# Kernel optimization log

Hardware: AMD Instinct MI355X
Metric: run time of the kernel (lower is better)

Reference implementation:

```python
import jax, jax.numpy as jnp
import numpy as np

FEAT = 128
BATCH = 4
T_VAL = 256
TAU_VAL = 256
N_NODES = T_VAL + TAU_VAL
NUM_SAMPLES = 5


def _linear_init(key, fan_in, fan_out):
    s = 1.0 / np.sqrt(fan_in)
    kw, kb = jax.random.split(key)
    W = jax.random.uniform(kw, (fan_in, fan_out), minval=-s, maxval=s, dtype=jnp.float32)
    b = jax.random.uniform(kb, (fan_out,), minval=-s, maxval=s, dtype=jnp.float32)
    return W, b


def setup_inputs() -> dict:
    key = jax.random.key(0)
    k0, k1, k2, k3 = jax.random.split(key, 4)
    W1, b1 = _linear_init(k0, 2 * FEAT, FEAT)
    W2, b2 = _linear_init(k1, FEAT, FEAT)
    W3, b3 = _linear_init(k2, FEAT, 1)
    nodes = jax.random.normal(k3, (BATCH, N_NODES, FEAT), dtype=jnp.float32)
    return dict(
        nodes=nodes,
        W1=W1, b1=b1, g1=jnp.ones((FEAT,), jnp.float32), be1=jnp.zeros((FEAT,), jnp.float32),
        W2=W2, b2=b2, g2=jnp.ones((FEAT,), jnp.float32), be2=jnp.zeros((FEAT,), jnp.float32),
        W3=W3, b3=b3,
        T=T_VAL, taus=TAU_VAL, B=BATCH,
    )


def _layernorm(h, g, b):
    mu = h.mean(-1, keepdims=True)
    var = ((h - mu) ** 2).mean(-1, keepdims=True)
    return (h - mu) / jnp.sqrt(var + 1e-5) * g + b


def reference(nodes, W1, b1, g1, be1, W2, b2, g2, be2, W3, b3, T, taus, B):
    N = nodes.shape[1]  # = T + taus
    # Static tril edge structure (uniform T, taus across batch): rows=sink, cols=source
    rows, cols = np.tril_indices(N, -1)
    keep = rows > T  # strictly greater, as in the torch code
    sink_idx = jnp.asarray(rows[keep])   # [E]
    src_idx = jnp.asarray(cols[keep])    # [E]
    E = sink_idx.shape[0]

    # Gather node pairs -> [B, E, 2F]
    net_in = jnp.concatenate([nodes[:, sink_idx], nodes[:, src_idx]], axis=-1)

    # Small MLP: Linear-ReLU-LN x2 + Linear -> logits [B, E]
    h = _layernorm(jax.nn.relu(net_in @ W1 + b1), g1, be1)
    h = _layernorm(jax.nn.relu(h @ W2 + b2), g2, be2)
    logits = (h @ W3 + b3)[..., 0]

    # Gumbel-softmax (hard, tau=1) over edges, NUM_SAMPLES samples per batch
    gkey = jax.random.key(42)
    gnoise = jax.random.gumbel(gkey, (logits.shape[0], NUM_SAMPLES, E), dtype=logits.dtype)
    y_soft = jax.nn.softmax(logits[:, None, :] + gnoise, axis=-1)  # [B, S, E]
    y_hard = jax.nn.one_hot(jnp.argmax(y_soft, axis=-1), E, dtype=y_soft.dtype)
    y = y_hard + y_soft - jax.lax.stop_gradient(y_soft)  # straight-through hard sample

    counts = y.sum(axis=1)  # [B, E], in [0, S]
    # StraightThroughEstimator: forward binarize >0, identity gradient
    path = (counts > 0).astype(counts.dtype) + counts - jax.lax.stop_gradient(counts)

    # Scatter into dense adjacency (dense form of the sparse COO output)
    bidx = jnp.arange(nodes.shape[0])[:, None]
    adj = jnp.zeros((nodes.shape[0], N, N), nodes.dtype)
    adj = adj.at[bidx, sink_idx[None, :], src_idx[None, :]].set(path)
    return adj
```

## Files before the change

kernel.cpp:

```cpp
#include <hip/hip_runtime.h>
#include <stdint.h>

#define FEAT 128
#define NNODES 512
#define BATCH 4
#define EDGES 97920
#define BE (BATCH*EDGES)
#define NSAMP 5
#define BASE_OFF 32896
#define CHUNKS 40
#define NWT (BE/32)
#define MLP_GRID 510
#define MAP_BLOCKS 383
#define PREP_BLOCKS 64
#define VEC_BLOCK (256 + MAP_BLOCKS + PREP_BLOCKS)
#define ZERO_BLOCKS 256
#define SETUP_GRID (VEC_BLOCK + 1 + ZERO_BLOCKS)

typedef float f32x4 __attribute__((ext_vector_type(4)));
typedef short s16x8 __attribute__((ext_vector_type(8)));

__device__ __forceinline__ void threefry2x32(uint32_t k0, uint32_t k1,
                                             uint32_t& x0, uint32_t& x1) {
  uint32_t k2 = k0 ^ k1 ^ 0x1BD11BDAu;
  x0 += k0; x1 += k1;
#define RR(r) { x0 += x1; x1 = (x1 << (r)) | (x1 >> (32 - (r))); x1 ^= x0; }
  RR(13) RR(15) RR(26) RR(6)   x0 += k1; x1 += k2 + 1u;
  RR(17) RR(29) RR(16) RR(24)  x0 += k2; x1 += k0 + 2u;
  RR(13) RR(15) RR(26) RR(6)   x0 += k0; x1 += k1 + 3u;
  RR(17) RR(29) RR(16) RR(24)  x0 += k1; x1 += k2 + 4u;
  RR(13) RR(15) RR(26) RR(6)   x0 += k2; x1 += k0 + 5u;
#undef RR
}

__device__ __forceinline__ float gumbel_valf(uint32_t n) {
  uint32_t x0 = 0u, x1 = n;
  threefry2x32(0u, 42u, x0, x1);
  uint32_t bits = x0 ^ x1;
  uint32_t fb = (bits >> 9) | 0x3f800000u;
  float f = __uint_as_float(fb) - 1.0f;
  float u = fmaxf(f, 1.1754943508222875e-38f);
  return -logf(-logf(u));
}

template <int CTRL>
__device__ __forceinline__ float dpp_ror_add(float v) {
  int t = __builtin_amdgcn_update_dpp(0, __float_as_int(v), CTRL, 0xF, 0xF, true);
  return v + __int_as_float(t);
}
__device__ __forceinline__ float row_sum16(float v) {
  v = dpp_ror_add<0x128>(v);
  v = dpp_ror_add<0x124>(v);
  v = dpp_ror_add<0x122>(v);
  v = dpp_ror_add<0x121>(v);
  return v;
}

__global__ __launch_bounds__(256) void setup_kernel(
    const float* __restrict__ nodes, const float* __restrict__ W1,
    const float* __restrict__ b1, const float* __restrict__ W2,
    const float* __restrict__ g1, const float* __restrict__ be1,
    const float* __restrict__ b2, const float* __restrict__ g2,
    const float* __restrict__ be2, const float* __restrict__ W3,
    const float* __restrict__ b3, float* __restrict__ P, float* __restrict__ Q,
    int2* __restrict__ map, unsigned short* __restrict__ GFH,
    unsigned short* __restrict__ GFL, float* __restrict__ SG,
    float* __restrict__ SB, float* __restrict__ GW3, float* __restrict__ SC,
    float* __restrict__ adj) {
  const int blk = blockIdx.x;
  const int tid = threadIdx.x;
  if (blk < 256) {
    __shared__ float snode[8][FEAT];
    const int row0 = blk * 8;
    for (int i = tid; i < 8 * FEAT; i += 256)
      snode[i >> 7][i & 127] = nodes[row0 * FEAT + i];
    __syncthreads();
    const int j = tid & 127;
    const int half = tid >> 7;
    const float* w = W1 + half * FEAT * FEAT + j;
    float acc[8] = {0, 0, 0, 0, 0, 0, 0, 0};
    for (int k4 = 0; k4 < 32; ++k4) {
      const float* wp = w + (k4 * 4) * FEAT;
      const float w0 = wp[0], w1 = wp[FEAT], w2 = wp[2 * FEAT], w3 = wp[3 * FEAT];
#pragma unroll
      for (int m = 0; m < 8; ++m) {
        const float4 nv = *(const float4*)&snode[m][k4 * 4];
        acc[m] = fmaf(nv.x, w0, acc[m]);
        acc[m] = fmaf(nv.y, w1, acc[m]);
        acc[m] = fmaf(nv.z, w2, acc[m]);
        acc[m] = fmaf(nv.w, w3, acc[m]);
      }
    }
    const float bv = half ? 0.0f : b1[j];
    float* out = half ? Q : P;
#pragma unroll
    for (int m = 0; m < 8; ++m) out[(row0 + m) * FEAT + j] = acc[m] + bv;
  } else if (blk < 256 + MAP_BLOCKS) {
    int e = (blk - 256) * 256 + tid;
    if (e < EDGES) {
      double x = (double)(e + BASE_OFF);
      int s = (int)((1.0 + sqrt(1.0 + 8.0 * x)) * 0.5);
      while ((long long)s * (s - 1) / 2 - BASE_OFF > e) --s;
      while ((long long)(s + 1) * s / 2 - BASE_OFF <= e) ++s;
      int src = e - (int)((long long)s * (s - 1) / 2 - BASE_OFF);
      map[e] = make_int2(s, src);
    }
  } else if (blk < VEC_BLOCK) {
    const int idx = (blk - (256 + MAP_BLOCKS)) * 256 + tid;
    const int j = idx & 7;
    const int lane = (idx >> 3) & 63;
    const int nt = (idx >> 9) & 7;
    const int kt = (idx >> 12) & 3;
    const int n = nt * 16 + (lane & 15);
    const int k = kt * 32 + ((lane >> 4) << 3) + j;
    const float g = g1[k] * W2[k * FEAT + n];
    const uint32_t gu = __float_as_uint(g);
    const float d = g - __uint_as_float(gu & 0xFFFF0000u);
    GFH[idx] = (unsigned short)(gu >> 16);
    GFL[idx] = (unsigned short)(__float_as_uint(d) >> 16);
  } else if (blk == VEC_BLOCK) {
    __shared__ float partS[256], partB[256], rg[128], rb[128];
    {
      const int n = tid & 127, kh = tid >> 7;
      float sg = 0.f, sb = 0.f;
      const int k0 = kh * 64;
#pragma unroll 8
      for (int k = k0; k < k0 + 64; ++k) {
        const float w = W2[k * FEAT + n];
        sg = fmaf(g1[k], w, sg);
        sb = fmaf(be1[k], w, sb);
      }
      partS[tid] = sg;
      partB[tid] = sb;
    }
    __syncthreads();
    if (tid < 128) {
      SG[tid] = partS[tid] + partS[tid + 128];
      SB[tid] = partB[tid] + partB[tid + 128] + b2[tid];
      const float gw = g2[tid] * W3[tid];
      GW3[tid] = gw;
      rg[tid] = gw;
      rb[tid] = be2[tid] * W3[tid];
    }
    __syncthreads();
    for (int off = 64; off; off >>= 1) {
      if (tid < off) { rg[tid] += rg[tid + off]; rb[tid] += rb[tid + off]; }
      __syncthreads();
    }
    if (tid == 0) { SC[0] = rg[0]; SC[1] = rb[0] + b3[0]; }
  } else {
    float4* a4 = (float4*)adj;
    const int base = (blk - (VEC_BLOCK + 1)) * 1024 + tid;
#pragma unroll
    for (int jj = 0; jj < 4; ++jj)
      a4[base + jj * 256] = make_float4(0.f, 0.f, 0.f, 0.f);
  }
}

__global__ __launch_bounds__(256, 2) void mlp_kernel(
    const float* __restrict__ P, const float* __restrict__ Q,
    const int2* __restrict__ map,
    const unsigned short* __restrict__ GFH,
    const unsigned short* __restrict__ GFL,
    const float* __restrict__ SG, const float* __restrict__ SB,
    const float* __restrict__ GW3, const float* __restrict__ SC,
    float* __restrict__ logits) {
  __shared__ s16x8 sBH[2048];
  __shared__ s16x8 sBL[2048];
  const int tid = threadIdx.x;
  const int lane = tid & 63;
  const int wave = tid >> 6;
  const int cl = lane & 15;
  const int qd = lane >> 4;

  {
    const float4* s1p = (const float4*)GFH;
    const float4* s2p = (const float4*)GFL;
    float4* d1 = (float4*)sBH;
    float4* d2 = (float4*)sBL;
    for (int i = tid; i < 2048; i += 256) { d1[i] = s1p[i]; d2[i] = s2p[i]; }
  }
  __syncthreads();

  const float sgw3 = SC[0], cb = SC[1];

#pragma unroll 1
  for (int it = 0; it < 6; ++it) {
    const int wt = blockIdx.x * 24 + it * 4 + wave;
    const int g0 = wt * 32;
    const int b = g0 / EDGES;
    const int e0 = g0 - b * EDGES;
    const int bofs = (b << 9);

    s16x8 Ah[2][4], Al[2][4];
    float s1v[2], q1v[2];
#pragma unroll
    for (int mt = 0; mt < 2; ++mt) {
      const int2 ss = map[e0 + mt * 16 + cl];
      const float* pr = P + ((size_t)(bofs + ss.x) << 7) + qd * 8;
      const float* qr = Q + ((size_t)(bofs + ss.y) << 7) + qd * 8;
      float s1 = 0.f, q1 = 0.f;
#pragma unroll
      for (int kt = 0; kt < 4; ++kt) {
        const float4 pa = *(const float4*)(pr + kt * 32);
        const float4 pb = *(const float4*)(pr + kt * 32 + 4);
        const float4 qa = *(const float4*)(qr + kt * 32);
        const float4 qb = *(const float4*)(qr + kt * 32 + 4);
        const float uu[8] = {
            fmaxf(pa.x + qa.x, 0.f), fmaxf(pa.y + qa.y, 0.f),
            fmaxf(pa.z + qa.z, 0.f), fmaxf(pa.w + qa.w, 0.f),
            fmaxf(pb.x + qb.x, 0.f), fmaxf(pb.y + qb.y, 0.f),
            fmaxf(pb.z + qb.z, 0.f), fmaxf(pb.w + qb.w, 0.f)};
#pragma unroll
        for (int j = 0; j < 8; ++j) {
          const float h = uu[j];
          s1 += h;
          q1 = fmaf(h, h, q1);
          const uint32_t xu = __float_as_uint(h);
          const float d = h - __uint_as_float(xu & 0xFFFF0000u);
          Ah[mt][kt][j] = (short)(xu >> 16);
          Al[mt][kt][j] = (short)(__float_as_uint(d) >> 16);
        }
      }
      s1v[mt] = s1;
      q1v[mt] = q1;
    }
    __builtin_amdgcn_sched_barrier(0);

    f32x4 acc[2][8];
#pragma unroll
    for (int mt = 0; mt < 2; ++mt)
#pragma unroll
      for (int nt = 0; nt < 8; ++nt) acc[mt][nt] = (f32x4){0.f, 0.f, 0.f, 0.f};

    s16x8 Bh[2][2], Bl[2][2];
#pragma unroll
    for (int s = 0; s < 2; ++s) {
      const int base = ((s >> 2) * 8 + (s & 3) * 2) * 64 + lane;
      Bh[s][0] = sBH[base];      Bl[s][0] = sBL[base];
      Bh[s][1] = sBH[base + 64]; Bl[s][1] = sBL[base + 64];
    }
#pragma unroll
    for (int g = 0; g < 16; ++g) {
      const int kt = g >> 2;
      const int n0 = (g & 3) * 2, n1 = n0 + 1;
      const int sl = g & 1;
      acc[0][n0] = __builtin_amdgcn_mfma_f32_16x16x32_bf16(Ah[0][kt], Bh[sl][0], acc[0][n0], 0, 0, 0);
      acc[1][n0] = __builtin_amdgcn_mfma_f32_16x16x32_bf16(Ah[1][kt], Bh[sl][0], acc[1][n0], 0, 0, 0);
      acc[0][n1] = __builtin_amdgcn_mfma_f32_16x16x32_bf16(Ah[0][kt], Bh[sl][1], acc[0][n1], 0, 0, 0);
      acc[1][n1] = __builtin_amdgcn_mfma_f32_16x16x32_bf16(Ah[1][kt], Bh[sl][1], acc[1][n1], 0, 0, 0);
      acc[0][n0] = __builtin_amdgcn_mfma_f32_16x16x32_bf16(Al[0][kt], Bh[sl][0], acc[0][n0], 0, 0, 0);
      acc[1][n0] = __builtin_amdgcn_mfma_f32_16x16x32_bf16(Al[1][kt], Bh[sl][0], acc[1][n0], 0, 0, 0);
      acc[0][n1] = __builtin_amdgcn_mfma_f32_16x16x32_bf16(Al[0][kt], Bh[sl][1], acc[0][n1], 0, 0, 0);
      acc[1][n1] = __builtin_amdgcn_mfma_f32_16x16x32_bf16(Al[1][kt], Bh[sl][1], acc[1][n1], 0, 0, 0);
      acc[0][n0] = __builtin_amdgcn_mfma_f32_16x16x32_bf16(Ah[0][kt], Bl[sl][0], acc[0][n0], 0, 0, 0);
      acc[1][n0] = __builtin_amdgcn_mfma_f32_16x16x32_bf16(Ah[1][kt], Bl[sl][0], acc[1][n0], 0, 0, 0);
      acc[0][n1] = __builtin_amdgcn_mfma_f32_16x16x32_bf16(Ah[0][kt], Bl[sl][1], acc[0][n1], 0, 0, 0);
      acc[1][n1] = __builtin_amdgcn_mfma_f32_16x16x32_bf16(Ah[1][kt], Bl[sl][1], acc[1][n1], 0, 0, 0);
      if (g < 14) {
        const int g2 = g + 2;
        const int base = ((g2 >> 2) * 8 + (g2 & 3) * 2) * 64 + lane;
        Bh[sl][0] = sBH[base];      Bl[sl][0] = sBL[base];
        Bh[sl][1] = sBH[base + 64]; Bl[sl][1] = sBL[base + 64];
      }
      __builtin_amdgcn_sched_barrier(0);
    }

    float mu[2], rs[2];
#pragma unroll
    for (int mt = 0; mt < 2; ++mt) {
      float s1 = s1v[mt], q1 = q1v[mt];
      s1 += __shfl_xor(s1, 16, 64);
      s1 += __shfl_xor(s1, 32, 64);
      q1 += __shfl_xor(q1, 16, 64);
      q1 += __shfl_xor(q1, 32, 64);
      mu[mt] = s1 * (1.0f / 128.0f);
      const float var = fmaxf(q1 * (1.0f / 128.0f) - mu[mt] * mu[mt], 0.0f);
      rs[mt] = rsqrtf(var + 1e-5f);
    }

    int zz;
    asm volatile("v_mov_b32 %0, 0" : "=v"(zz));
    float SGn[8], SBn[8], GWn[8];
#pragma unroll
    for (int nt = 0; nt < 8; ++nt) {
      const int n = nt * 16 + cl + zz;
      SGn[nt] = SG[n];
      SBn[nt] = SB[n];
      GWn[nt] = GW3[n];
    }
#pragma unroll
    for (int mt = 0; mt < 2; ++mt) {
#pragma unroll
      for (int r = 0; r < 4; ++r) {
        const int me = qd * 4 + r;
        const float mue = __shfl(mu[mt], me, 64);
        const float rse = __shfl(rs[mt], me, 64);
        float s2 = 0.f, q2 = 0.f, t = 0.f;
#pragma unroll
        for (int nt = 0; nt < 8; ++nt) {
          const float Sraw = acc[mt][nt][r];
          const float z = fmaf(rse, fmaf(-mue, SGn[nt], Sraw), SBn[nt]);
          const float h2 = fmaxf(z, 0.f);
          s2 += h2;
          q2 = fmaf(h2, h2, q2);
          t = fmaf(h2, GWn[nt], t);
        }
        s2 = row_sum16(s2);
        q2 = row_sum16(q2);
        t  = row_sum16(t);
        if (cl == 0) {
          const float mu2 = s2 * (1.0f / 128.0f);
          const float var2 = fmaxf(q2 * (1.0f / 128.0f) - mu2 * mu2, 0.0f);
          const float rs2 = rsqrtf(var2 + 1e-5f);
          logits[g0 + mt * 16 + me] = rs2 * (t - mu2 * sgw3) + cb;
        }
      }
    }
  }
}

__global__ __launch_bounds__(256) void gumbel_kernel(
    const float* __restrict__ logits, float* __restrict__ bestval,
    int* __restrict__ bestidx) {
  const int bs = blockIdx.x / CHUNKS;
  const int chunk = blockIdx.x % CHUNKS;
  const int b = bs / NSAMP;
  const float* lg = logits + b * EDGES;
  float best = -1e30f; int bi = 0x7fffffff;
  for (int e = chunk * 256 + threadIdx.x; e < EDGES; e += CHUNKS * 256) {
    uint32_t n = (uint32_t)(bs * EDGES + e);
    float val = lg[e] + gumbel_valf(n);
    if (val > best) { best = val; bi = e; }
  }
  __shared__ float sv[256];
  __shared__ int si[256];
  sv[threadIdx.x] = best; si[threadIdx.x] = bi;
  __syncthreads();
  for (int off = 128; off; off >>= 1) {
    if (threadIdx.x < off) {
      float ov = sv[threadIdx.x + off]; int oi = si[threadIdx.x + off];
      if (ov > sv[threadIdx.x] ||
          (ov == sv[threadIdx.x] && oi < si[threadIdx.x])) {
        sv[threadIdx.x] = ov; si[threadIdx.x] = oi;
      }
    }
    __syncthreads();
  }
  if (threadIdx.x == 0) { bestval[blockIdx.x] = sv[0]; bestidx[blockIdx.x] = si[0]; }
}

__global__ __launch_bounds__(64) void select_kernel(
    const float* __restrict__ bestval, const int* __restrict__ bestidx,
    const int2* __restrict__ map, float* __restrict__ adj) {
  const int bs = blockIdx.x;
  const int lane = threadIdx.x;
  float v = -1e30f; int idx = 0x7fffffff;
  if (lane < CHUNKS) { v = bestval[bs * CHUNKS + lane]; idx = bestidx[bs * CHUNKS + lane]; }
#pragma unroll
  for (int off = 32; off; off >>= 1) {
    float ov = __shfl_xor(v, off, 64);
    int oi = __shfl_xor(idx, off, 64);
    if (ov > v || (ov == v && oi < idx)) { v = ov; idx = oi; }
  }
  if (lane == 0) {
    int b = bs / NSAMP;
    int2 ss = map[idx];
    adj[((b * NNODES) + ss.x) * NNODES + ss.y] = 1.0f;
  }
}

extern "C" void kernel_launch(void* const* d_in, const int* in_sizes, int n_in,
                              void* d_out, int out_size, void* d_ws, size_t ws_size,
                              hipStream_t stream) {
  const float* nodes = (const float*)d_in[0];
  const float* W1  = (const float*)d_in[1];
  const float* b1  = (const float*)d_in[2];
  const float* g1  = (const float*)d_in[3];
  const float* be1 = (const float*)d_in[4];
  const float* W2  = (const float*)d_in[5];
  const float* b2  = (const float*)d_in[6];
  const float* g2  = (const float*)d_in[7];
  const float* be2 = (const float*)d_in[8];
  const float* W3  = (const float*)d_in[9];
  const float* b3  = (const float*)d_in[10];
  float* adj = (float*)d_out;

  char* ws = (char*)d_ws;
  float* P       = (float*)(ws);
  float* Q       = (float*)(ws + (1 << 20));
  int2*  map     = (int2*) (ws + (2 << 20));
  float* logits  = (float*)(ws + (3 << 20));
  unsigned short* GFH = (unsigned short*)(ws + (5 << 20));
  unsigned short* GFL = (unsigned short*)(ws + (5 << 20) + 32768);
  float* SG      = (float*)(ws + (5 << 20) + 65536);
  float* SB      = (float*)(ws + (5 << 20) + 66048);
  float* GW3     = (float*)(ws + (5 << 20) + 66560);
  float* SC      = (float*)(ws + (5 << 20) + 67072);
  float* bestval = (float*)(ws + (5 << 20) + 131072);
  int*   bestidx = (int*)  (ws + (5 << 20) + 137472);

  setup_kernel<<<SETUP_GRID, 256, 0, stream>>>(
      nodes, W1, b1, W2, g1, be1, b2, g2, be2, W3, b3,
      P, Q, map, GFH, GFL, SG, SB, GW3, SC, adj);
  mlp_kernel<<<MLP_GRID, 256, 0, stream>>>(P, Q, map, GFH, GFL,
                                           SG, SB, GW3, SC, logits);
  gumbel_kernel<<<20 * CHUNKS, 256, 0, stream>>>(logits, bestval, bestidx);
  select_kernel<<<20, 64, 0, stream>>>(bestval, bestidx, map, adj);
}
```

Baseline: 153.1 us.

## Shrink MLP wave tile to 16 edges, read low-part weights from global

Each wave now handles 16 edges per iteration instead of 32, with twice as many iterations per block. This halves the register footprint and allows occupancy hint 3. The low bf16 half of the weight matrix is no longer staged in LDS and is instead loaded directly from global memory, which halves shared memory use per block. The trade-off is less B-operand reuse per wave, since each weight fragment now feeds half as many MFMAs, plus extra global or L2 traffic for the low-part weights inside the MFMA loop.

Result: slower. 240.9 us (+57.4%).

```diff
diff --git a/kernel.cpp b/kernel.cpp
--- a/kernel.cpp
+++ b/kernel.cpp
@@ -9,7 +9,7 @@
 #define NSAMP 5
 #define BASE_OFF 32896
 #define CHUNKS 40
-#define NWT (BE/32)
+#define NWT (BE/16)
 #define MLP_GRID 510
 #define MAP_BLOCKS 383
 #define PREP_BLOCKS 64
@@ -157,7 +157,7 @@
   }
 }
 
-__global__ __launch_bounds__(256, 2) void mlp_kernel(
+__global__ __launch_bounds__(256, 3) void mlp_kernel(
     const float* __restrict__ P, const float* __restrict__ Q,
     const int2* __restrict__ map,
     const unsigned short* __restrict__ GFH,
@@ -166,7 +166,6 @@
     const float* __restrict__ GW3, const float* __restrict__ SC,
     float* __restrict__ logits) {
   __shared__ s16x8 sBH[2048];
-  __shared__ s16x8 sBL[2048];
   const int tid = threadIdx.x;
   const int lane = tid & 63;
   const int wave = tid >> 6;
@@ -175,31 +174,28 @@
 
   {
     const float4* s1p = (const float4*)GFH;
-    const float4* s2p = (const float4*)GFL;
     float4* d1 = (float4*)sBH;
-    float4* d2 = (float4*)sBL;
-    for (int i = tid; i < 2048; i += 256) { d1[i] = s1p[i]; d2[i] = s2p[i]; }
+    for (int i = tid; i < 2048; i += 256) d1[i] = s1p[i];
   }
   __syncthreads();
 
+  const s16x8* gfl = (const s16x8*)GFL;
   const float sgw3 = SC[0], cb = SC[1];
 
 #pragma unroll 1
-  for (int it = 0; it < 6; ++it) {
-    const int wt = blockIdx.x * 24 + it * 4 + wave;
-    const int g0 = wt * 32;
+  for (int it = 0; it < 12; ++it) {
+    const int wt = blockIdx.x * 48 + it * 4 + wave;
+    const int g0 = wt * 16;
     const int b = g0 / EDGES;
     const int e0 = g0 - b * EDGES;
     const int bofs = (b << 9);
 
-    s16x8 Ah[2][4], Al[2][4];
-    float s1v[2], q1v[2];
-#pragma unroll
-    for (int mt = 0; mt < 2; ++mt) {
-      const int2 ss = map[e0 + mt * 16 + cl];
+    s16x8 Ah[4], Al[4];
+    float s1 = 0.f, q1 = 0.f;
+    {
+      const int2 ss = map[e0 + cl];
       const float* pr = P + ((size_t)(bofs + ss.x) << 7) + qd * 8;
       const float* qr = Q + ((size_t)(bofs + ss.y) << 7) + qd * 8;
-      float s1 = 0.f, q1 = 0.f;
 #pragma unroll
       for (int kt = 0; kt < 4; ++kt) {
         const float4 pa = *(const float4*)(pr + kt * 32);
@@ -218,66 +214,51 @@
           q1 = fmaf(h, h, q1);
           const uint32_t xu = __float_as_uint(h);
           const float d = h - __uint_as_float(xu & 0xFFFF0000u);
-          Ah[mt][kt][j] = (short)(xu >> 16);
-          Al[mt][kt][j] = (short)(__float_as_uint(d) >> 16);
+          Ah[kt][j] = (short)(xu >> 16);
+          Al[kt][j] = (short)(__float_as_uint(d) >> 16);
         }
       }
-      s1v[mt] = s1;
-      q1v[mt] = q1;
     }
     __builtin_amdgcn_sched_barrier(0);
 
-    f32x4 acc[2][8];
-#pragma unroll
-    for (int mt = 0; mt < 2; ++mt)
-#pragma unroll
-      for (int nt = 0; nt < 8; ++nt) acc[mt][nt] = (f32x4){0.f, 0.f, 0.f, 0.f};
+    f32x4 acc[8];
+#pragma unroll
+    for (int nt = 0; nt < 8; ++nt) acc[nt] = (f32x4){0.f, 0.f, 0.f, 0.f};
 
     s16x8 Bh[2][2], Bl[2][2];
 #pragma unroll
     for (int s = 0; s < 2; ++s) {
       const int base = ((s >> 2) * 8 + (s & 3) * 2) * 64 + lane;
-      Bh[s][0] = sBH[base];      Bl[s][0] = sBL[base];
-      Bh[s][1] = sBH[base + 64]; Bl[s][1] = sBL[base + 64];
+      Bh[s][0] = sBH[base];      Bl[s][0] = gfl[base];
+      Bh[s][1] = sBH[base + 64]; Bl[s][1] = gfl[base + 64];
     }
 #pragma unroll
     for (int g = 0; g < 16; ++g) {
       const int kt = g >> 2;
       const int n0 = (g & 3) * 2, n1 = n0 + 1;
       const int sl = g & 1;
-      acc[0][n0] = __builtin_amdgcn_mfma_f32_16x16x32_bf16(Ah[0][kt], Bh[sl][0], acc[0][n0], 0, 0, 0);
-      acc[1][n0] = __builtin_amdgcn_mfma_f32_16x16x32_bf16(Ah[1][kt], Bh[sl][0], acc[1][n0], 0, 0, 0);
-      acc[0][n1] = __builtin_amdgcn_mfma_f32_16x16x32_bf16(Ah[0][kt], Bh[sl][1], acc[0][n1], 0, 0, 0);
-      acc[1][n1] = __builtin_amdgcn_mfma_f32_16x16x32_bf16(Ah[1][kt], Bh[sl][1], acc[1][n1], 0, 0, 0);
-      acc[0][n0] = __builtin_amdgcn_mfma_f32_16x16x32_bf16(Al[0][kt], Bh[sl][0], acc[0][n0], 0, 0, 0);
-      acc[1][n0] = __builtin_amdgcn_mfma_f32_16x16x32_bf16(Al[1][kt], Bh[sl][0], acc[1][n0], 0, 0, 0);
-      acc[0][n1] = __builtin_amdgcn_mfma_f32_16x16x32_bf16(Al[0][kt], Bh[sl][1], acc[0][n1], 0, 0, 0);
-      acc[1][n1] = __builtin_amdgcn_mfma_f32_16x16x32_bf16(Al[1][kt], Bh[sl][1], acc[1][n1], 0, 0, 0);
-      acc[0][n0] = __builtin_amdgcn_mfma_f32_16x16x32_bf16(Ah[0][kt], Bl[sl][0], acc[0][n0], 0, 0, 0);
-      acc[1][n0] = __builtin_amdgcn_mfma_f32_16x16x32_bf16(Ah[1][kt], Bl[sl][0], acc[1][n0], 0, 0, 0);
-      acc[0][n1] = __builtin_amdgcn_mfma_f32_16x16x32_bf16(Ah[0][kt], Bl[sl][1], acc[0][n1], 0, 0, 0);
-      acc[1][n1] = __builtin_amdgcn_mfma_f32_16x16x32_bf16(Ah[1][kt], Bl[sl][1], acc[1][n1], 0, 0, 0);
+      acc[n0] = __builtin_amdgcn_mfma_f32_16x16x32_bf16(Ah[kt], Bh[sl][0], acc[n0], 0, 0, 0);
+      acc[n1] = __builtin_amdgcn_mfma_f32_16x16x32_bf16(Ah[kt], Bh[sl][1], acc[n1], 0, 0, 0);
+      acc[n0] = __builtin_amdgcn_mfma_f32_16x16x32_bf16(Al[kt], Bh[sl][0], acc[n0], 0, 0, 0);
+      acc[n1] = __builtin_amdgcn_mfma_f32_16x16x32_bf16(Al[kt], Bh[sl][1], acc[n1], 0, 0, 0);
+      acc[n0] = __builtin_amdgcn_mfma_f32_16x16x32_bf16(Ah[kt], Bl[sl][0], acc[n0], 0, 0, 0);
+      acc[n1] = __builtin_amdgcn_mfma_f32_16x16x32_bf16(Ah[kt], Bl[sl][1], acc[n1], 0, 0, 0);
       if (g < 14) {
         const int g2 = g + 2;
         const int base = ((g2 >> 2) * 8 + (g2 & 3) * 2) * 64 + lane;
-        Bh[sl][0] = sBH[base];      Bl[sl][0] = sBL[base];
-        Bh[sl][1] = sBH[base + 64]; Bl[sl][1] = sBL[base + 64];
+        Bh[sl][0] = sBH[base];      Bl[sl][0] = gfl[base];
+        Bh[sl][1] = sBH[base + 64]; Bl[sl][1] = gfl[base + 64];
       }
       __builtin_amdgcn_sched_barrier(0);
     }
 
-    float mu[2], rs[2];
-#pragma unroll
-    for (int mt = 0; mt < 2; ++mt) {
-      float s1 = s1v[mt], q1 = q1v[mt];
-      s1 += __shfl_xor(s1, 16, 64);
-      s1 += __shfl_xor(s1, 32, 64);
-      q1 += __shfl_xor(q1, 16, 64);
-      q1 += __shfl_xor(q1, 32, 64);
-      mu[mt] = s1 * (1.0f / 128.0f);
-      const float var = fmaxf(q1 * (1.0f / 128.0f) - mu[mt] * mu[mt], 0.0f);
-      rs[mt] = rsqrtf(var + 1e-5f);
-    }
+    s1 += __shfl_xor(s1, 16, 64);
+    s1 += __shfl_xor(s1, 32, 64);
+    q1 += __shfl_xor(q1, 16, 64);
+    q1 += __shfl_xor(q1, 32, 64);
+    const float mu = s1 * (1.0f / 128.0f);
+    const float var = fmaxf(q1 * (1.0f / 128.0f) - mu * mu, 0.0f);
+    const float rs = rsqrtf(var + 1e-5f);
 
     int zz;
     asm volatile("v_mov_b32 %0, 0" : "=v"(zz));
@@ -290,31 +271,28 @@
       GWn[nt] = GW3[n];
     }
 #pragma unroll
-    for (int mt = 0; mt < 2; ++mt) {
-#pragma unroll
-      for (int r = 0; r < 4; ++r) {
-        const int me = qd * 4 + r;
-        const float mue = __shfl(mu[mt], me, 64);
-        const float rse = __shfl(rs[mt], me, 64);
-        float s2 = 0.f, q2 = 0.f, t = 0.f;
-#pragma unroll
-        for (int nt = 0; nt < 8; ++nt) {
-          const float Sraw = acc[mt][nt][r];
-          const float z = fmaf(rse, fmaf(-mue, SGn[nt], Sraw), SBn[nt]);
-          const float h2 = fmaxf(z, 0.f);
-          s2 += h2;
-          q2 = fmaf(h2, h2, q2);
-          t = fmaf(h2, GWn[nt], t);
-        }
-        s2 = row_sum16(s2);
-        q2 = row_sum16(q2);
-        t  = row_sum16(t);
-        if (cl == 0) {
-          const float mu2 = s2 * (1.0f / 128.0f);
-          const float var2 = fmaxf(q2 * (1.0f / 128.0f) - mu2 * mu2, 0.0f);
-          const float rs2 = rsqrtf(var2 + 1e-5f);
-          logits[g0 + mt * 16 + me] = rs2 * (t - mu2 * sgw3) + cb;
-        }
+    for (int r = 0; r < 4; ++r) {
+      const int me = qd * 4 + r;
+      const float mue = __shfl(mu, me, 64);
+      const float rse = __shfl(rs, me, 64);
+      float s2 = 0.f, q2 = 0.f, t = 0.f;
+#pragma unroll
+      for (int nt = 0; nt < 8; ++nt) {
+        const float Sraw = acc[nt][r];
+        const float z = fmaf(rse, fmaf(-mue, SGn[nt], Sraw), SBn[nt]);
+        const float h2 = fmaxf(z, 0.f);
+        s2 += h2;
+        q2 = fmaf(h2, h2, q2);
+        t = fmaf(h2, GWn[nt], t);
+      }
+      s2 = row_sum16(s2);
+      q2 = row_sum16(q2);
+      t  = row_sum16(t);
+      if (cl == 0) {
+        const float mu2 = s2 * (1.0f / 128.0f);
+        const float var2 = fmaxf(q2 * (1.0f / 128.0f) - mu2 * mu2, 0.0f);
+        const float rs2 = rsqrtf(var2 + 1e-5f);
+        logits[g0 + me] = rs2 * (t - mu2 * sgw3) + cb;
       }
     }
   }
```
